# Performance work log

Measured on AMD Instinct MI355X. Metric: run time of the kernel, lower is better.

Reference implementation:

```python
import jax, jax.numpy as jnp
import numpy as np

N_NODES = 100000
N_EDGES = 3200000
NFEAT, NHID, OPFEAT = 128, 128, 64
EPS = 1e-06


def setup_inputs() -> dict:
    key = jax.random.key(0)
    ks = jax.random.split(key, 20)
    def u(k, shape, s):
        return jax.random.uniform(k, shape, jnp.float32, -s, s)
    inp = {
        'x': jax.random.normal(ks[0], (N_NODES, NFEAT), jnp.float32),
        'edge_rows': jax.random.randint(ks[1], (N_EDGES,), 0, N_NODES, jnp.int32),
        'edge_cols': jax.random.randint(ks[2], (N_EDGES,), 0, N_NODES, jnp.int32),
        'edge_vals': jax.random.uniform(ks[3], (N_EDGES,), jnp.float32),
        # fc layers (torch Linear: weight [out, in])
        'fc1_w': u(ks[4], (NHID, NFEAT), 1.0 / np.sqrt(NFEAT)),
        'fc1_b': u(ks[5], (NHID,), 1.0 / np.sqrt(NFEAT)),
        'fc2_w': u(ks[6], (NHID, NHID), 1.0 / np.sqrt(NHID)),
        'fc2_b': u(ks[7], (NHID,), 1.0 / np.sqrt(NHID)),
        'ln_gamma': jnp.ones((NHID,), jnp.float32),
        'ln_beta': jnp.zeros((NHID,), jnp.float32),
    }
    s = 1.0 / np.sqrt(NHID)
    for i, out_f in zip(range(1, 5), [NHID, NHID, NHID, OPFEAT]):
        k1, k2, k3 = jax.random.split(jax.random.fold_in(key, 100 + i), 3)
        inp[f'gc{i}_wn'] = u(k1, (NHID, out_f), s)
        inp[f'gc{i}_ws'] = u(k2, (NHID, out_f), s)
        inp[f'gc{i}_b'] = u(k3, (out_f,), s)
    return inp


def _gcn_first_order(x, wn, ws, b, rows, cols, vals):
    # act_self + sparse_adj @ (x @ wn) + bias
    act_self = x @ ws                      # [N, out]
    support = x @ wn                       # [N, out]
    gathered = support[cols] * vals[:, None]   # [E, out] irregular gather
    act_neighbor = jax.ops.segment_sum(gathered, rows, num_segments=x.shape[0])
    return act_self + act_neighbor + b


def _layer_norm(x, gamma, beta):
    mean = jnp.mean(x, axis=-1, keepdims=True)
    std = jnp.std(x, axis=-1, keepdims=True, ddof=1)  # torch .std is unbiased
    return gamma * (x - mean) / (std + EPS) + beta


def reference(x, edge_rows, edge_cols, edge_vals,
              fc1_w, fc1_b, fc2_w, fc2_b, ln_gamma, ln_beta,
              gc1_wn, gc1_ws, gc1_b, gc2_wn, gc2_ws, gc2_b,
              gc3_wn, gc3_ws, gc3_b, gc4_wn, gc4_ws, gc4_b):
    h = jax.nn.relu(x @ fc1_w.T + fc1_b)
    h = jax.nn.relu(h @ fc2_w.T + fc2_b)
    h = _layer_norm(h, ln_gamma, ln_beta)
    h = jax.nn.relu(_gcn_first_order(h, gc1_wn, gc1_ws, gc1_b, edge_rows, edge_cols, edge_vals))
    h = jax.nn.relu(_gcn_first_order(h, gc2_wn, gc2_ws, gc2_b, edge_rows, edge_cols, edge_vals))
    h = jax.nn.relu(_gcn_first_order(h, gc3_wn, gc3_ws, gc3_b, edge_rows, edge_cols, edge_vals))
    h = jax.nn.relu(_gcn_first_order(h, gc4_wn, gc4_ws, gc4_b, edge_rows, edge_cols, edge_vals))
    return h
```

## Files before the change

kernel.cpp:

```cpp
#include <hip/hip_runtime.h>

constexpr int N_NODES = 100000;
constexpr int N_EDGES = 3200000;
constexpr float EPS = 1e-6f;

constexpr int NBKT = 196;
constexpr int BKT_SHIFT = 9;
constexpr int BKT_ROWS = 512;
constexpr int ARENA_STRIDE = 18432;
constexpr int EPB1 = 8000;
constexpr int NBLK1 = 400;
constexpr int CAP = 72;

typedef __attribute__((ext_vector_type(8))) short bfrag;
typedef __attribute__((ext_vector_type(4))) float ffrag;

__device__ __forceinline__ unsigned short f2bf(float f) {
    unsigned int u = __float_as_uint(f);
    u += 0x7FFFu + ((u >> 16) & 1u);
    return (unsigned short)(u >> 16);
}
__device__ __forceinline__ float bf_lo(unsigned int w) { return __uint_as_float(w << 16); }
__device__ __forceinline__ float bf_hi(unsigned int w) { return __uint_as_float(w & 0xFFFF0000u); }

#define FMA8(v_, s_)                                                          \
    acc[0] = fmaf(v_, bf_lo(s_.x), acc[0]); acc[1] = fmaf(v_, bf_hi(s_.x), acc[1]); \
    acc[2] = fmaf(v_, bf_lo(s_.y), acc[2]); acc[3] = fmaf(v_, bf_hi(s_.y), acc[3]); \
    acc[4] = fmaf(v_, bf_lo(s_.z), acc[4]); acc[5] = fmaf(v_, bf_hi(s_.z), acc[5]); \
    acc[6] = fmaf(v_, bf_lo(s_.w), acc[6]); acc[7] = fmaf(v_, bf_hi(s_.w), acc[7]);

__global__ __launch_bounds__(256) void prep_w_k(
    const float* __restrict__ fc1_w, const float* __restrict__ fc2_w,
    const float* __restrict__ wn0, const float* __restrict__ ws0,
    const float* __restrict__ wn1, const float* __restrict__ ws1,
    const float* __restrict__ wn2, const float* __restrict__ ws2,
    const float* __restrict__ wn3, const float* __restrict__ ws3,
    unsigned short* __restrict__ Wb)
{
    int idx = blockIdx.x * 256 + threadIdx.x;
    if (idx >= 147456) return;
    float v;
    if (idx < 32768) {
        int r = idx >> 7, k = idx & 127;
        v = (r < 128) ? fc1_w[r * 128 + k] : fc2_w[(r - 128) * 128 + k];
    } else if (idx < 131072) {
        int idx2 = idx - 32768;
        int l = idx2 >> 15, w = idx2 & 32767;
        int o = w >> 8, k = w & 255;
        const float* wn = l == 0 ? wn0 : l == 1 ? wn1 : wn2;
        const float* ws = l == 0 ? ws0 : l == 1 ? ws1 : ws2;
        v = (k < 128) ? ws[k * 128 + o] : wn[(k - 128) * 128 + o];
    } else {
        int idx3 = idx - 131072;
        int o = idx3 >> 7, k = idx3 & 127;
        v = (o < 64) ? wn3[k * 64 + o] : ws3[k * 64 + (o - 64)];
    }
    Wb[idx] = f2bf(v);
}

__global__ __launch_bounds__(256) void front_k(
    const int* __restrict__ rows, const int* __restrict__ cols,
    const float* __restrict__ vals, int* gcur,
    unsigned* __restrict__ arena_e, unsigned short* __restrict__ arena_r,
    const float* __restrict__ x, const float* __restrict__ fc1_w,
    const float* __restrict__ fc1_b, unsigned short* __restrict__ Yb)
{
    __shared__ __align__(16) char smem[59136];
    const int tid = threadIdx.x;

    if (blockIdx.x < NBLK1) {
        int* hist   = (int*)smem;
        int* lstart = hist + NBKT;
        int* lcur   = lstart + NBKT;
        int* gbase  = lcur + NBKT;
        unsigned* st_e        = (unsigned*)(gbase + NBKT);
        unsigned short* st_r  = (unsigned short*)(st_e + EPB1);
        unsigned char* st_b   = (unsigned char*)(st_r + EPB1);
        const int e0 = blockIdx.x * EPB1;
        const int ecnt = min(EPB1, N_EDGES - e0);

        for (int i = tid; i < NBKT; i += 256) hist[i] = 0;
        __syncthreads();
        for (int i = tid; i < ecnt; i += 256)
            atomicAdd(&hist[rows[e0 + i] >> BKT_SHIFT], 1);
        __syncthreads();
        if (tid == 0) {
            int s = 0;
            for (int b = 0; b < NBKT; b++) { lstart[b] = s; s += hist[b]; }
        }
        __syncthreads();
        for (int i = tid; i < NBKT; i += 256) lcur[i] = lstart[i];
        __syncthreads();
        for (int i = tid; i < ecnt; i += 256) {
            int r = rows[e0 + i];
            int b = r >> BKT_SHIFT;
            unsigned entry = ((unsigned)cols[e0 + i] << 15)
                           | (unsigned)(f2bf(vals[e0 + i]) & 0x7FFF);
            int pos = atomicAdd(&lcur[b], 1);
            st_e[pos] = entry;
            st_r[pos] = (unsigned short)(r & (BKT_ROWS - 1));
            st_b[pos] = (unsigned char)b;
        }
        __syncthreads();
        for (int b = tid; b < NBKT; b += 256) {
            int cnt = lcur[b] - lstart[b];
            gbase[b] = cnt > 0 ? atomicAdd(&gcur[b], cnt) : 0;
        }
        __syncthreads();
        for (int i = tid; i < ecnt; i += 256) {
            int b = st_b[i];
            int off = gbase[b] + (i - lstart[b]);
            if (off < ARENA_STRIDE) {
                long dest = (long)b * ARENA_STRIDE + off;
                arena_e[dest] = st_e[i];
                arena_r[dest] = st_r[i];
            }
        }
        return;
    }

    unsigned short* Bs = (unsigned short*)smem;
    for (int i = tid; i < 16384; i += 256) {
        int n = i >> 7, k = i & 127;
        Bs[n * 136 + k] = f2bf(fc1_w[i]);
    }
    const int wave = tid >> 6, lane = tid & 63;
    const int quad = lane >> 4, l16 = lane & 15;
    const long base = (long)(blockIdx.x - NBLK1) * 128 + wave * 32;

    union AU { uint4 q; bfrag v; unsigned short s[8]; };
    bfrag a[2][4];
#pragma unroll
    for (int mt = 0; mt < 2; mt++) {
        long node = base + mt * 16 + l16;
        bool ok = node < N_NODES;
        const float4* Ar = (const float4*)(x + node * 128);
#pragma unroll
        for (int t = 0; t < 4; t++) {
            AU u;
            if (ok) {
                float4 f0 = Ar[t * 8 + quad * 2];
                float4 f1 = Ar[t * 8 + quad * 2 + 1];
                u.s[0] = f2bf(f0.x); u.s[1] = f2bf(f0.y);
                u.s[2] = f2bf(f0.z); u.s[3] = f2bf(f0.w);
                u.s[4] = f2bf(f1.x); u.s[5] = f2bf(f1.y);
                u.s[6] = f2bf(f1.z); u.s[7] = f2bf(f1.w);
            } else u.q = make_uint4(0, 0, 0, 0);
            a[mt][t] = u.v;
        }
    }
    __syncthreads();

    ffrag acc[2][8];
#pragma unroll
    for (int mt = 0; mt < 2; mt++)
#pragma unroll
        for (int nt = 0; nt < 8; nt++) acc[mt][nt] = (ffrag)0.f;

#pragma unroll
    for (int t = 0; t < 4; t++)
#pragma unroll
        for (int nt = 0; nt < 8; nt++) {
            bfrag b = *(const bfrag*)&Bs[(nt * 16 + l16) * 136 + t * 32 + quad * 8];
            acc[0][nt] = __builtin_amdgcn_mfma_f32_16x16x32_bf16(a[0][t], b, acc[0][nt], 0, 0, 0);
            acc[1][nt] = __builtin_amdgcn_mfma_f32_16x16x32_bf16(a[1][t], b, acc[1][nt], 0, 0, 0);
        }

    float bv[8];
#pragma unroll
    for (int nt = 0; nt < 8; nt++) bv[nt] = fc1_b[nt * 16 + l16];
#pragma unroll
    for (int mt = 0; mt < 2; mt++)
#pragma unroll
        for (int reg = 0; reg < 4; reg++) {
            long node = base + mt * 16 + quad * 4 + reg;
            if (node >= N_NODES) continue;
#pragma unroll
            for (int nt = 0; nt < 8; nt++)
                Yb[node * 128 + nt * 16 + l16] = f2bf(fmaxf(acc[mt][nt][reg] + bv[nt], 0.f));
        }
}

template<int MODE>
__global__ __launch_bounds__(256, 2) void mfma_gemm_k(
    const void* Av, const unsigned short* __restrict__ Wg_,
    const float* __restrict__ bias,
    const float* __restrict__ gamma, const float* __restrict__ beta,
    unsigned short* __restrict__ Yb, float* Tout)
{
    constexpr int NT = 8;
    __shared__ unsigned short Bs[128 * 136];
    const int tid = threadIdx.x;

    const uint4* Wg = (const uint4*)Wg_;
    uint4* Bs4 = (uint4*)Bs;
    for (int i = tid; i < 128 * 16; i += 256) {
        int n = i >> 4, c = i & 15;
        Bs4[n * 17 + c] = Wg[i];
    }

    const int wave = tid >> 6, lane = tid & 63;
    const int quad = lane >> 4, l16 = lane & 15;
    const long base = (long)blockIdx.x * 128 + wave * 32;

    union AU { uint4 q; bfrag v; };
    bfrag a[2][4];
#pragma unroll
    for (int mt = 0; mt < 2; mt++) {
        long node = base + mt * 16 + l16;
        bool ok = node < N_NODES;
        const uint4* Ar = (const uint4*)((const unsigned short*)Av + node * 128);
#pragma unroll
        for (int t = 0; t < 4; t++) {
            AU u;
            u.q = ok ? Ar[t * 4 + quad] : make_uint4(0, 0, 0, 0);
            a[mt][t] = u.v;
        }
    }
    __syncthreads();

    ffrag acc[2][NT];
#pragma unroll
    for (int mt = 0; mt < 2; mt++)
#pragma unroll
        for (int nt = 0; nt < NT; nt++) acc[mt][nt] = (ffrag)0.f;

#pragma unroll
    for (int t = 0; t < 4; t++)
#pragma unroll
        for (int nt = 0; nt < NT; nt++) {
            bfrag b = *(const bfrag*)&Bs[(nt * 16 + l16) * 136 + t * 32 + quad * 8];
            acc[0][nt] = __builtin_amdgcn_mfma_f32_16x16x32_bf16(a[0][t], b, acc[0][nt], 0, 0, 0);
            acc[1][nt] = __builtin_amdgcn_mfma_f32_16x16x32_bf16(a[1][t], b, acc[1][nt], 0, 0, 0);
        }

    if (MODE == 1) {
        float bv[NT], gv[NT], bev[NT];
#pragma unroll
        for (int nt = 0; nt < NT; nt++) {
            bv[nt] = bias[nt * 16 + l16];
            gv[nt] = gamma[nt * 16 + l16];
            bev[nt] = beta[nt * 16 + l16];
        }
#pragma unroll
        for (int mt = 0; mt < 2; mt++)
#pragma unroll
            for (int reg = 0; reg < 4; reg++) {
                long node = base + mt * 16 + quad * 4 + reg;
                if (node >= N_NODES) continue;
                float v[NT], s = 0.f, sq = 0.f;
#pragma unroll
                for (int nt = 0; nt < NT; nt++) {
                    v[nt] = fmaxf(acc[mt][nt][reg] + bv[nt], 0.f);
                    s += v[nt]; sq += v[nt] * v[nt];
                }
#pragma unroll
                for (int off = 1; off < 16; off <<= 1) {
                    s  += __shfl_xor(s, off, 64);
                    sq += __shfl_xor(sq, off, 64);
                }
                float mean = s * (1.f / 128.f);
                float var = fmaxf((sq - 128.f * mean * mean) * (1.f / 127.f), 0.f);
                float inv = 1.f / (sqrtf(var) + EPS);
#pragma unroll
                for (int nt = 0; nt < NT; nt++)
                    Yb[node * 128 + nt * 16 + l16] = f2bf(gv[nt] * (v[nt] - mean) * inv + bev[nt]);
            }
    } else {
        float bv[4];
#pragma unroll
        for (int i = 0; i < 4; i++) bv[i] = bias[i * 16 + l16];
#pragma unroll
        for (int mt = 0; mt < 2; mt++)
#pragma unroll
            for (int reg = 0; reg < 4; reg++) {
                long node = base + mt * 16 + quad * 4 + reg;
                if (node >= N_NODES) continue;
#pragma unroll
                for (int nt = 0; nt < 4; nt++)
                    Yb[node * 64 + nt * 16 + l16] = f2bf(acc[mt][nt][reg]);
#pragma unroll
                for (int nt = 4; nt < 8; nt++)
                    Tout[node * 64 + (nt - 4) * 16 + l16] = acc[mt][nt][reg] + bv[nt - 4];
            }
    }
}

__global__ __launch_bounds__(256, 2) void fused_gemm_k(
    const unsigned short* __restrict__ A1, const unsigned short* __restrict__ A2,
    const unsigned short* __restrict__ Wg_, const float* __restrict__ bias,
    unsigned short* __restrict__ Y)
{
    constexpr int NT = 8;
    __shared__ unsigned short Bs[128 * 264];
    const int tid = threadIdx.x;

    const uint4* Wg = (const uint4*)Wg_;
    uint4* Bs4 = (uint4*)Bs;
    for (int i = tid; i < 128 * 32; i += 256) {
        int n = i >> 5, c = i & 31;
        Bs4[n * 33 + c] = Wg[i];
    }

    const int wave = tid >> 6, lane = tid & 63;
    const int quad = lane >> 4, l16 = lane & 15;
    const long base = (long)blockIdx.x * 128 + wave * 32;

    union AU { uint4 q; bfrag v; };
    bfrag a[2][8];
#pragma unroll
    for (int mt = 0; mt < 2; mt++) {
        long node = base + mt * 16 + l16;
        bool ok = node < N_NODES;
        const uint4* A1r = (const uint4*)(A1 + node * 128);
        const uint4* A2r = (const uint4*)(A2 + node * 128);
#pragma unroll
        for (int t = 0; t < 4; t++) {
            AU u1, u2;
            u1.q = ok ? A1r[t * 4 + quad] : make_uint4(0, 0, 0, 0);
            u2.q = ok ? A2r[t * 4 + quad] : make_uint4(0, 0, 0, 0);
            a[mt][t] = u1.v;
            a[mt][4 + t] = u2.v;
        }
    }
    __syncthreads();

    ffrag acc[2][NT];
#pragma unroll
    for (int mt = 0; mt < 2; mt++)
#pragma unroll
        for (int nt = 0; nt < NT; nt++) acc[mt][nt] = (ffrag)0.f;

#pragma unroll
    for (int t = 0; t < 8; t++)
#pragma unroll
        for (int nt = 0; nt < NT; nt++) {
            bfrag b = *(const bfrag*)&Bs[(nt * 16 + l16) * 264 + t * 32 + quad * 8];
            acc[0][nt] = __builtin_amdgcn_mfma_f32_16x16x32_bf16(a[0][t], b, acc[0][nt], 0, 0, 0);
            acc[1][nt] = __builtin_amdgcn_mfma_f32_16x16x32_bf16(a[1][t], b, acc[1][nt], 0, 0, 0);
        }

    float bv[NT];
#pragma unroll
    for (int nt = 0; nt < NT; nt++) bv[nt] = bias[nt * 16 + l16];
#pragma unroll
    for (int mt = 0; mt < 2; mt++)
#pragma unroll
        for (int reg = 0; reg < 4; reg++) {
            long node = base + mt * 16 + quad * 4 + reg;
            if (node >= N_NODES) continue;
#pragma unroll
            for (int nt = 0; nt < NT; nt++)
                Y[node * 128 + nt * 16 + l16] = f2bf(fmaxf(acc[mt][nt][reg] + bv[nt], 0.f));
        }
}

__global__ __launch_bounds__(1024) void build_k(
    const int* __restrict__ gcur, const unsigned* __restrict__ arena_e,
    const unsigned short* __restrict__ arena_r,
    unsigned* __restrict__ csr, int* __restrict__ cursor)
{
    __shared__ int cnt[BKT_ROWS];
    const int tid = threadIdx.x;
    const int b = blockIdx.x;
    for (int i = tid; i < BKT_ROWS; i += 1024) cnt[i] = 0;
    __syncthreads();
    const int ec = min(gcur[b], ARENA_STRIDE);
    const long abase = (long)b * ARENA_STRIDE;
    for (int i = tid; i < ec; i += 1024) {
        unsigned entry = arena_e[abase + i];
        int rib = arena_r[abase + i] & (BKT_ROWS - 1);
        int rank = atomicAdd(&cnt[rib], 1);
        if (rank < CAP)
            csr[((long)b * BKT_ROWS + rib) * CAP + rank] = entry;
    }
    __syncthreads();
    for (int i = tid; i < BKT_ROWS; i += 1024) {
        int gr = b * BKT_ROWS + i;
        if (gr < N_NODES) cursor[gr] = min(cnt[i], CAP);
    }
}

__global__ __launch_bounds__(256) void gather_k(
    const int* __restrict__ cursor, const unsigned* __restrict__ csr,
    const unsigned short* __restrict__ Sb, unsigned short* __restrict__ G)
{
    int node = blockIdx.x * 4 + (threadIdx.x >> 6);
    if (node >= N_NODES) return;
    int lane = threadIdx.x & 63;
    int fl = lane & 15, ep = lane >> 4;
    const long s = (long)node * CAP;
    const int total = min(cursor[node], CAP);

    float acc[8] = {0, 0, 0, 0, 0, 0, 0, 0};
    const uint4* S4 = (const uint4*)Sb;

    for (int base = 0; base < total; base += 64) {
        int idx = base + lane;
        unsigned ed = (idx < total) ? csr[s + idx] : 0u;
        int cnt = total - base; if (cnt > 64) cnt = 64;
        const int U0 = cnt >> 4;
        int j = ep, u = 0;
        for (; u + 2 <= U0; u += 2, j += 32) {
            unsigned p0 = (unsigned)__shfl((int)ed, j, 64);
            unsigned p1 = (unsigned)__shfl((int)ed, j + 4, 64);
            unsigned p2 = (unsigned)__shfl((int)ed, j + 8, 64);
            unsigned p3 = (unsigned)__shfl((int)ed, j + 12, 64);
            unsigned p4 = (unsigned)__shfl((int)ed, j + 16, 64);
            unsigned p5 = (unsigned)__shfl((int)ed, j + 20, 64);
            unsigned p6 = (unsigned)__shfl((int)ed, j + 24, 64);
            unsigned p7 = (unsigned)__shfl((int)ed, j + 28, 64);
            uint4 s0 = S4[((p0 >> 15) << 4) + fl];
            uint4 s1 = S4[((p1 >> 15) << 4) + fl];
            uint4 s2 = S4[((p2 >> 15) << 4) + fl];
            uint4 s3 = S4[((p3 >> 15) << 4) + fl];
            uint4 s4 = S4[((p4 >> 15) << 4) + fl];
            uint4 s5 = S4[((p5 >> 15) << 4) + fl];
            uint4 s6 = S4[((p6 >> 15) << 4) + fl];
            uint4 s7 = S4[((p7 >> 15) << 4) + fl];
            float v0 = __uint_as_float((p0 & 0x7FFFu) << 16);
            float v1 = __uint_as_float((p1 & 0x7FFFu) << 16);
            float v2 = __uint_as_float((p2 & 0x7FFFu) << 16);
            float v3 = __uint_as_float((p3 & 0x7FFFu) << 16);
            float v4 = __uint_as_float((p4 & 0x7FFFu) << 16);
            float v5 = __uint_as_float((p5 & 0x7FFFu) << 16);
            float v6 = __uint_as_float((p6 & 0x7FFFu) << 16);
            float v7 = __uint_as_float((p7 & 0x7FFFu) << 16);
            FMA8(v0, s0) FMA8(v1, s1) FMA8(v2, s2) FMA8(v3, s3)
            FMA8(v4, s4) FMA8(v5, s5) FMA8(v6, s6) FMA8(v7, s7)
        }
        if (u < U0) {
            unsigned p0 = (unsigned)__shfl((int)ed, j, 64);
            unsigned p1 = (unsigned)__shfl((int)ed, j + 4, 64);
            unsigned p2 = (unsigned)__shfl((int)ed, j + 8, 64);
            unsigned p3 = (unsigned)__shfl((int)ed, j + 12, 64);
            uint4 s0 = S4[((p0 >> 15) << 4) + fl];
            uint4 s1 = S4[((p1 >> 15) << 4) + fl];
            uint4 s2 = S4[((p2 >> 15) << 4) + fl];
            uint4 s3 = S4[((p3 >> 15) << 4) + fl];
            float v0 = __uint_as_float((p0 & 0x7FFFu) << 16);
            float v1 = __uint_as_float((p1 & 0x7FFFu) << 16);
            float v2 = __uint_as_float((p2 & 0x7FFFu) << 16);
            float v3 = __uint_as_float((p3 & 0x7FFFu) << 16);
            FMA8(v0, s0) FMA8(v1, s1) FMA8(v2, s2) FMA8(v3, s3)
            j += 16;
        }
        int T = (cnt - (U0 << 4) + 3) >> 2;
        for (int t = 0; t < T; t++, j += 4) {
            unsigned p0 = (unsigned)__shfl((int)ed, j, 64);
            float v0 = __uint_as_float((p0 & 0x7FFFu) << 16);
            uint4 s0 = S4[((p0 >> 15) << 4) + fl];
            FMA8(v0, s0)
        }
    }
#pragma unroll
    for (int off = 16; off < 64; off <<= 1)
#pragma unroll
        for (int j = 0; j < 8; j++) acc[j] += __shfl_xor(acc[j], off, 64);

    if (ep == 0) {
        uint4 p;
        p.x = (unsigned)f2bf(acc[0]) | ((unsigned)f2bf(acc[1]) << 16);
        p.y = (unsigned)f2bf(acc[2]) | ((unsigned)f2bf(acc[3]) << 16);
        p.z = (unsigned)f2bf(acc[4]) | ((unsigned)f2bf(acc[5]) << 16);
        p.w = (unsigned)f2bf(acc[6]) | ((unsigned)f2bf(acc[7]) << 16);
        ((uint4*)G)[node * 16 + fl] = p;
    }
}

__global__ __launch_bounds__(256) void gather64_k(
    const int* __restrict__ cursor, const unsigned* __restrict__ csr,
    const unsigned short* __restrict__ Sb, const float* __restrict__ T,
    float* __restrict__ out)
{
    int node = blockIdx.x * 4 + (threadIdx.x >> 6);
    if (node >= N_NODES) return;
    int lane = threadIdx.x & 63;
    int fl = lane & 7, ep = lane >> 3;
    const long s = (long)node * CAP;
    const int total = min(cursor[node], CAP);

    float acc[8] = {0, 0, 0, 0, 0, 0, 0, 0};
    const uint4* S4 = (const uint4*)Sb;

    for (int base = 0; base < total; base += 64) {
        int idx = base + lane;
        unsigned ed = (idx < total) ? csr[s + idx] : 0u;
        int cnt = total - base; if (cnt > 64) cnt = 64;
        const int U0 = cnt >> 4;
        int j = ep, u = 0;
        for (; u + 2 <= U0; u += 2, j += 32) {
            unsigned p0 = (unsigned)__shfl((int)ed, j, 64);
            unsigned p1 = (unsigned)__shfl((int)ed, j + 8, 64);
            unsigned p2 = (unsigned)__shfl((int)ed, j + 16, 64);
            unsigned p3 = (unsigned)__shfl((int)ed, j + 24, 64);
            uint4 s0 = S4[((p0 >> 15) << 3) + fl];
            uint4 s1 = S4[((p1 >> 15) << 3) + fl];
            uint4 s2 = S4[((p2 >> 15) << 3) + fl];
            uint4 s3 = S4[((p3 >> 15) << 3) + fl];
            float v0 = __uint_as_float((p0 & 0x7FFFu) << 16);
            float v1 = __uint_as_float((p1 & 0x7FFFu) << 16);
            float v2 = __uint_as_float((p2 & 0x7FFFu) << 16);
            float v3 = __uint_as_float((p3 & 0x7FFFu) << 16);
            FMA8(v0, s0) FMA8(v1, s1) FMA8(v2, s2) FMA8(v3, s3)
        }
        if (u < U0) {
            unsigned p0 = (unsigned)__shfl((int)ed, j, 64);
            unsigned p1 = (unsigned)__shfl((int)ed, j + 8, 64);
            uint4 s0 = S4[((p0 >> 15) << 3) + fl];
            uint4 s1 = S4[((p1 >> 15) << 3) + fl];
            float v0 = __uint_as_float((p0 & 0x7FFFu) << 16);
            float v1 = __uint_as_float((p1 & 0x7FFFu) << 16);
            FMA8(v0, s0) FMA8(v1, s1)
            j += 16;
        }
        int TT = (cnt - (U0 << 4) + 7) >> 3;
        for (int t = 0; t < TT; t++, j += 8) {
            unsigned p0 = (unsigned)__shfl((int)ed, j, 64);
            float v0 = __uint_as_float((p0 & 0x7FFFu) << 16);
            uint4 s0 = S4[((p0 >> 15) << 3) + fl];
            FMA8(v0, s0)
        }
    }
#pragma unroll
    for (int off = 8; off < 64; off <<= 1)
#pragma unroll
        for (int j = 0; j < 8; j++) acc[j] += __shfl_xor(acc[j], off, 64);

    if (ep == 0) {
        const float4* T4 = (const float4*)T;
        float4 t0 = T4[(long)node * 16 + fl * 2];
        float4 t1 = T4[(long)node * 16 + fl * 2 + 1];
        float4 o0, o1;
        o0.x = fmaxf(acc[0] + t0.x, 0.f); o0.y = fmaxf(acc[1] + t0.y, 0.f);
        o0.z = fmaxf(acc[2] + t0.z, 0.f); o0.w = fmaxf(acc[3] + t0.w, 0.f);
        o1.x = fmaxf(acc[4] + t1.x, 0.f); o1.y = fmaxf(acc[5] + t1.y, 0.f);
        o1.z = fmaxf(acc[6] + t1.z, 0.f); o1.w = fmaxf(acc[7] + t1.w, 0.f);
        ((float4*)out)[(long)node * 16 + fl * 2]     = o0;
        ((float4*)out)[(long)node * 16 + fl * 2 + 1] = o1;
    }
}

extern "C" void kernel_launch(void* const* d_in, const int* in_sizes, int n_in,
                              void* d_out, int out_size, void* d_ws, size_t ws_size,
                              hipStream_t stream)
{
    const float* x     = (const float*)d_in[0];
    const int*   erows = (const int*)d_in[1];
    const int*   ecols = (const int*)d_in[2];
    const float* evals = (const float*)d_in[3];
    const float* fc1_w = (const float*)d_in[4];
    const float* fc1_b = (const float*)d_in[5];
    const float* fc2_w = (const float*)d_in[6];
    const float* fc2_b = (const float*)d_in[7];
    const float* ln_g  = (const float*)d_in[8];
    const float* ln_b  = (const float*)d_in[9];
    const float* gc_wn[4] = {(const float*)d_in[10], (const float*)d_in[13],
                             (const float*)d_in[16], (const float*)d_in[19]};
    const float* gc_ws[4] = {(const float*)d_in[11], (const float*)d_in[14],
                             (const float*)d_in[17], (const float*)d_in[20]};
    const float* gc_b[4]  = {(const float*)d_in[12], (const float*)d_in[15],
                             (const float*)d_in[18], (const float*)d_in[21]};

    unsigned short* Abf = (unsigned short*)d_ws;
    unsigned short* Gbf = Abf + (size_t)N_NODES * 128;
    unsigned* csr = (unsigned*)(Gbf + (size_t)N_NODES * 128);
    unsigned* arena_e = csr + (size_t)N_NODES * CAP;
    unsigned short* arena_r =
        (unsigned short*)(arena_e + (size_t)NBKT * ARENA_STRIDE);
    unsigned short* Wb = arena_r + (size_t)NBKT * ARENA_STRIDE;
    int* cursor = (int*)(Wb + 147456);
    int* gcur   = cursor + N_NODES;
    float* Tf   = (float*)Abf;
    float* out = (float*)d_out;

    dim3 blk(256);
    int gemm_grid = (N_NODES + 127) / 128;
    int node_grid = (N_NODES + 3) / 4;

    hipMemsetAsync(gcur, 0, NBKT * 4, stream);
    front_k<<<NBLK1 + gemm_grid, blk, 0, stream>>>(
        erows, ecols, evals, gcur, arena_e, arena_r,
        x, fc1_w, fc1_b, Gbf);

    prep_w_k<<<(147456 + 255) / 256, blk, 0, stream>>>(
        fc1_w, fc2_w, gc_wn[0], gc_ws[0], gc_wn[1], gc_ws[1],
        gc_wn[2], gc_ws[2], gc_wn[3], gc_ws[3], Wb);

    build_k<<<NBKT, dim3(1024), 0, stream>>>(gcur, arena_e, arena_r, csr, cursor);

    mfma_gemm_k<1><<<gemm_grid, blk, 0, stream>>>(
        Gbf, Wb + 16384, fc2_b, ln_g, ln_b, Abf, nullptr);

    for (int l = 0; l < 3; l++) {
        gather_k<<<node_grid, blk, 0, stream>>>(cursor, csr, Abf, Gbf);
        fused_gemm_k<<<gemm_grid, blk, 0, stream>>>(
            Abf, Gbf, Wb + 32768 + l * 32768, gc_b[l], Abf);
    }

    mfma_gemm_k<2><<<gemm_grid, blk, 0, stream>>>(
        Abf, Wb + 131072, gc_b[3], nullptr, nullptr, Gbf, Tf);
    gather64_k<<<node_grid, blk, 0, stream>>>(cursor, csr, Gbf, Tf, out);
}
```

Baseline: 721.7 us.

## Use 512-thread blocks for fused GEMM and reduce gather unrolling

```diff
diff --git a/kernel.cpp b/kernel.cpp
--- a/kernel.cpp
+++ b/kernel.cpp
@@ -286,7 +286,7 @@
     }
 }
 
-__global__ __launch_bounds__(256, 2) void fused_gemm_k(
+__global__ __launch_bounds__(512, 1) void fused_gemm_k(
     const unsigned short* __restrict__ A1, const unsigned short* __restrict__ A2,
     const unsigned short* __restrict__ Wg_, const float* __restrict__ bias,
     unsigned short* __restrict__ Y)
@@ -297,14 +297,14 @@
 
     const uint4* Wg = (const uint4*)Wg_;
     uint4* Bs4 = (uint4*)Bs;
-    for (int i = tid; i < 128 * 32; i += 256) {
+    for (int i = tid; i < 128 * 32; i += 512) {
         int n = i >> 5, c = i & 31;
         Bs4[n * 33 + c] = Wg[i];
     }
 
     const int wave = tid >> 6, lane = tid & 63;
     const int quad = lane >> 4, l16 = lane & 15;
-    const long base = (long)blockIdx.x * 128 + wave * 32;
+    const long base = (long)blockIdx.x * 256 + wave * 32;
 
     union AU { uint4 q; bfrag v; };
     bfrag a[2][8];
@@ -399,53 +399,43 @@
         int idx = base + lane;
         unsigned ed = (idx < total) ? csr[s + idx] : 0u;
         int cnt = total - base; if (cnt > 64) cnt = 64;
-        const int U0 = cnt >> 4;
-        int j = ep, u = 0;
-        for (; u + 2 <= U0; u += 2, j += 32) {
+        int U = cnt >> 4;
+        int j = ep;
+        for (int u = 0; u < U; u++, j += 16) {
             unsigned p0 = (unsigned)__shfl((int)ed, j, 64);
             unsigned p1 = (unsigned)__shfl((int)ed, j + 4, 64);
             unsigned p2 = (unsigned)__shfl((int)ed, j + 8, 64);
             unsigned p3 = (unsigned)__shfl((int)ed, j + 12, 64);
-            unsigned p4 = (unsigned)__shfl((int)ed, j + 16, 64);
-            unsigned p5 = (unsigned)__shfl((int)ed, j + 20, 64);
-            unsigned p6 = (unsigned)__shfl((int)ed, j + 24, 64);
-            unsigned p7 = (unsigned)__shfl((int)ed, j + 28, 64);
+            float v0 = __uint_as_float((p0 & 0x7FFFu) << 16);
+            float v1 = __uint_as_float((p1 & 0x7FFFu) << 16);
+            float v2 = __uint_as_float((p2 & 0x7FFFu) << 16);
+            float v3 = __uint_as_float((p3 & 0x7FFFu) << 16);
             uint4 s0 = S4[((p0 >> 15) << 4) + fl];
             uint4 s1 = S4[((p1 >> 15) << 4) + fl];
             uint4 s2 = S4[((p2 >> 15) << 4) + fl];
             uint4 s3 = S4[((p3 >> 15) << 4) + fl];
-            uint4 s4 = S4[((p4 >> 15) << 4) + fl];
-            uint4 s5 = S4[((p5 >> 15) << 4) + fl];
-            uint4 s6 = S4[((p6 >> 15) << 4) + fl];
-            uint4 s7 = S4[((p7 >> 15) << 4) + fl];
-            float v0 = __uint_as_float((p0 & 0x7FFFu) << 16);
-            float v1 = __uint_as_float((p1 & 0x7FFFu) << 16);
-            float v2 = __uint_as_float((p2 & 0x7FFFu) << 16);
-            float v3 = __uint_as_float((p3 & 0x7FFFu) << 16);
-            float v4 = __uint_as_float((p4 & 0x7FFFu) << 16);
-            float v5 = __uint_as_float((p5 & 0x7FFFu) << 16);
-            float v6 = __uint_as_float((p6 & 0x7FFFu) << 16);
-            float v7 = __uint_as_float((p7 & 0x7FFFu) << 16);
-            FMA8(v0, s0) FMA8(v1, s1) FMA8(v2, s2) FMA8(v3, s3)
-            FMA8(v4, s4) FMA8(v5, s5) FMA8(v6, s6) FMA8(v7, s7)
-        }
-        if (u < U0) {
-            unsigned p0 = (unsigned)__shfl((int)ed, j, 64);
-            unsigned p1 = (unsigned)__shfl((int)ed, j + 4, 64);
-            unsigned p2 = (unsigned)__shfl((int)ed, j + 8, 64);
-            unsigned p3 = (unsigned)__shfl((int)ed, j + 12, 64);
-            uint4 s0 = S4[((p0 >> 15) << 4) + fl];
-            uint4 s1 = S4[((p1 >> 15) << 4) + fl];
-            uint4 s2 = S4[((p2 >> 15) << 4) + fl];
-            uint4 s3 = S4[((p3 >> 15) << 4) + fl];
-            float v0 = __uint_as_float((p0 & 0x7FFFu) << 16);
-            float v1 = __uint_as_float((p1 & 0x7FFFu) << 16);
-            float v2 = __uint_as_float((p2 & 0x7FFFu) << 16);
-            float v3 = __uint_as_float((p3 & 0x7FFFu) << 16);
-            FMA8(v0, s0) FMA8(v1, s1) FMA8(v2, s2) FMA8(v3, s3)
-            j += 16;
-        }
-        int T = (cnt - (U0 << 4) + 3) >> 2;
+            { float v = v0; uint4 q = s0; float* accp = acc; (void)accp;
+              acc[0] = fmaf(v, bf_lo(q.x), acc[0]); acc[1] = fmaf(v, bf_hi(q.x), acc[1]);
+              acc[2] = fmaf(v, bf_lo(q.y), acc[2]); acc[3] = fmaf(v, bf_hi(q.y), acc[3]);
+              acc[4] = fmaf(v, bf_lo(q.z), acc[4]); acc[5] = fmaf(v, bf_hi(q.z), acc[5]);
+              acc[6] = fmaf(v, bf_lo(q.w), acc[6]); acc[7] = fmaf(v, bf_hi(q.w), acc[7]); }
+            { float v = v1; uint4 q = s1;
+              acc[0] = fmaf(v, bf_lo(q.x), acc[0]); acc[1] = fmaf(v, bf_hi(q.x), acc[1]);
+              acc[2] = fmaf(v, bf_lo(q.y), acc[2]); acc[3] = fmaf(v, bf_hi(q.y), acc[3]);
+              acc[4] = fmaf(v, bf_lo(q.z), acc[4]); acc[5] = fmaf(v, bf_hi(q.z), acc[5]);
+              acc[6] = fmaf(v, bf_lo(q.w), acc[6]); acc[7] = fmaf(v, bf_hi(q.w), acc[7]); }
+            { float v = v2; uint4 q = s2;
+              acc[0] = fmaf(v, bf_lo(q.x), acc[0]); acc[1] = fmaf(v, bf_hi(q.x), acc[1]);
+              acc[2] = fmaf(v, bf_lo(q.y), acc[2]); acc[3] = fmaf(v, bf_hi(q.y), acc[3]);
+              acc[4] = fmaf(v, bf_lo(q.z), acc[4]); acc[5] = fmaf(v, bf_hi(q.z), acc[5]);
+              acc[6] = fmaf(v, bf_lo(q.w), acc[6]); acc[7] = fmaf(v, bf_hi(q.w), acc[7]); }
+            { float v = v3; uint4 q = s3;
+              acc[0] = fmaf(v, bf_lo(q.x), acc[0]); acc[1] = fmaf(v, bf_hi(q.x), acc[1]);
+              acc[2] = fmaf(v, bf_lo(q.y), acc[2]); acc[3] = fmaf(v, bf_hi(q.y), acc[3]);
+              acc[4] = fmaf(v, bf_lo(q.z), acc[4]); acc[5] = fmaf(v, bf_hi(q.z), acc[5]);
+              acc[6] = fmaf(v, bf_lo(q.w), acc[6]); acc[7] = fmaf(v, bf_hi(q.w), acc[7]); }
+        }
+        int T = (cnt - (U << 4) + 3) >> 2;
         for (int t = 0; t < T; t++, j += 4) {
             unsigned p0 = (unsigned)__shfl((int)ed, j, 64);
             float v0 = __uint_as_float((p0 & 0x7FFFu) << 16);
@@ -487,34 +477,18 @@
         int idx = base + lane;
         unsigned ed = (idx < total) ? csr[s + idx] : 0u;
         int cnt = total - base; if (cnt > 64) cnt = 64;
-        const int U0 = cnt >> 4;
-        int j = ep, u = 0;
-        for (; u + 2 <= U0; u += 2, j += 32) {
+        int U = cnt >> 4;
+        int j = ep;
+        for (int u = 0; u < U; u++, j += 16) {
             unsigned p0 = (unsigned)__shfl((int)ed, j, 64);
             unsigned p1 = (unsigned)__shfl((int)ed, j + 8, 64);
-            unsigned p2 = (unsigned)__shfl((int)ed, j + 16, 64);
-            unsigned p3 = (unsigned)__shfl((int)ed, j + 24, 64);
+            float v0 = __uint_as_float((p0 & 0x7FFFu) << 16);
+            float v1 = __uint_as_float((p1 & 0x7FFFu) << 16);
             uint4 s0 = S4[((p0 >> 15) << 3) + fl];
             uint4 s1 = S4[((p1 >> 15) << 3) + fl];
-            uint4 s2 = S4[((p2 >> 15) << 3) + fl];
-            uint4 s3 = S4[((p3 >> 15) << 3) + fl];
-            float v0 = __uint_as_float((p0 & 0x7FFFu) << 16);
-            float v1 = __uint_as_float((p1 & 0x7FFFu) << 16);
-            float v2 = __uint_as_float((p2 & 0x7FFFu) << 16);
-            float v3 = __uint_as_float((p3 & 0x7FFFu) << 16);
-            FMA8(v0, s0) FMA8(v1, s1) FMA8(v2, s2) FMA8(v3, s3)
-        }
-        if (u < U0) {
-            unsigned p0 = (unsigned)__shfl((int)ed, j, 64);
-            unsigned p1 = (unsigned)__shfl((int)ed, j + 8, 64);
-            uint4 s0 = S4[((p0 >> 15) << 3) + fl];
-            uint4 s1 = S4[((p1 >> 15) << 3) + fl];
-            float v0 = __uint_as_float((p0 & 0x7FFFu) << 16);
-            float v1 = __uint_as_float((p1 & 0x7FFFu) << 16);
             FMA8(v0, s0) FMA8(v1, s1)
-            j += 16;
-        }
-        int TT = (cnt - (U0 << 4) + 7) >> 3;
+        }
+        int TT = (cnt - (U << 4) + 7) >> 3;
         for (int t = 0; t < TT; t++, j += 8) {
             unsigned p0 = (unsigned)__shfl((int)ed, j, 64);
             float v0 = __uint_as_float((p0 & 0x7FFFu) << 16);
@@ -576,6 +550,7 @@
 
     dim3 blk(256);
     int gemm_grid = (N_NODES + 127) / 128;
+    int fg_grid   = (N_NODES + 255) / 256;
     int node_grid = (N_NODES + 3) / 4;
 
     hipMemsetAsync(gcur, 0, NBKT * 4, stream);
@@ -594,7 +569,7 @@
 
     for (int l = 0; l < 3; l++) {
         gather_k<<<node_grid, blk, 0, stream>>>(cursor, csr, Abf, Gbf);
-        fused_gemm_k<<<gemm_grid, blk, 0, stream>>>(
+        fused_gemm_k<<<fg_grid, dim3(512), 0, stream>>>(
             Abf, Gbf, Wb + 32768 + l * 32768, gc_b[l], Abf);
     }
 
```

Result: faster. 685.1 us (-5.1%).
